# Optimization experiments

Measured on AMD Instinct MI355X. Metric: run time of the kernel, lower is better.

## Reference

```python
import jax, jax.numpy as jnp
from jax import lax
import numpy as np

FS = 48000
N_CHANNELS = 40
LOW_FREQ = 50
BATCH = 8
T_SAMPLES = 96000  # 2 s at 48 kHz
DOWN_FACTOR = 24   # 48 kHz -> 2 kHz envelope rate


def make_erb_fcoefs(fs, n_channels, low_freq):
    """Port of make_ERB_filters (Slaney gammatone coefficients). (C, 10)."""
    T = 1.0 / fs
    EarQ, minBW = 9.26449, 24.7
    i = np.arange(1, n_channels + 1, dtype=np.float64)
    hi = fs / 2
    cf = -(EarQ * minBW) + np.exp(i * (-np.log(hi + EarQ * minBW) + np.log(low_freq + EarQ * minBW)) / n_channels) * (hi + EarQ * minBW)
    erb = cf / EarQ + minBW
    B = 1.019 * 2 * np.pi * erb
    c = np.cos(2 * cf * np.pi * T)
    s = np.sin(2 * cf * np.pi * T)
    e = np.exp(B * T)
    sp = np.sqrt(3 + 2 ** 1.5)
    sm = np.sqrt(3 - 2 ** 1.5)
    a0 = T
    b1 = -2 * c / e
    b2 = np.exp(-2 * B * T)
    a11 = -(2 * T * c / e + 2 * sp * T * s / e) / 2
    a12 = -(2 * T * c / e - 2 * sp * T * s / e) / 2
    a13 = -(2 * T * c / e + 2 * sm * T * s / e) / 2
    a14 = -(2 * T * c / e - 2 * sm * T * s / e) / 2
    z = np.exp(4j * cf * np.pi * T)
    w = np.exp(-(B * T) + 2j * cf * np.pi * T)
    gain = np.abs(
        (-2 * z * T + 2 * w * T * (c - sm * s)) *
        (-2 * z * T + 2 * w * T * (c + sm * s)) *
        (-2 * z * T + 2 * w * T * (c - sp * s)) *
        (-2 * z * T + 2 * w * T * (c + sp * s)) /
        (-2 / np.exp(2 * B * T) - 2 * z + 2 * (1 + z) / np.exp(B * T)) ** 4)
    fcoefs = np.stack([np.full_like(cf, a0), a11, a12, a13, a14,
                       np.zeros_like(cf), np.ones_like(cf), b1, b2, gain], axis=1)
    return fcoefs.astype(np.float32)


def setup_inputs() -> dict:
    key = jax.random.key(0)
    x = jax.random.normal(key, (BATCH, T_SAMPLES), dtype=jnp.float32)
    fcoefs = jnp.asarray(make_erb_fcoefs(FS, N_CHANNELS, LOW_FREQ))
    return {"x": x, "fcoefs": fcoefs}


def _erb_filter_bank(x, fcoefs):
    """Cascaded 4-stage biquad gammatone bank. x: (B, T) -> (B, C, T)."""
    C = fcoefs.shape[0]
    Bsz = x.shape[0]
    a0 = fcoefs[:, 0]
    a2 = fcoefs[:, 5]  # zeros
    gain = fcoefs[:, 9]
    # numerator coeffs per stage, (4, 3, C); stage 1 divided by gain
    num = jnp.stack([
        jnp.stack([a0 / gain, fcoefs[:, 1] / gain, a2 / gain]),
        jnp.stack([a0, fcoefs[:, 2], a2]),
        jnp.stack([a0, fcoefs[:, 3], a2]),
        jnp.stack([a0, fcoefs[:, 4], a2]),
    ])
    d1 = fcoefs[:, 7]  # denominator (b0 == 1)
    d2 = fcoefs[:, 8]

    def step(carry, xt):
        s1, s2 = carry  # each (4, B, C): DF-II-transposed states per stage
        xk = jnp.broadcast_to(xt[:, None], (Bsz, C))
        ns1, ns2 = [], []
        for k in range(4):
            y = num[k, 0] * xk + s1[k]
            ns1.append(num[k, 1] * xk - d1 * y + s2[k])
            ns2.append(num[k, 2] * xk - d2 * y)
            xk = y
        return (jnp.stack(ns1), jnp.stack(ns2)), xk

    s0 = jnp.zeros((4, Bsz, C), x.dtype)
    _, ys = lax.scan(step, (s0, s0), x.T)  # ys: (T, B, C)
    return jnp.transpose(ys, (1, 2, 0))    # (B, C, T)


def reference(x, fcoefs):
    sub = _erb_filter_bank(x, fcoefs)          # (B, C, T)
    sub = jax.nn.relu(sub)                      # half-wave rectification
    Bsz, C, T = sub.shape
    env = sub.reshape(Bsz, C, T // DOWN_FACTOR, DOWN_FACTOR).mean(-1)  # avg-pool downsample
    return env  # (B, C, T/DOWN_FACTOR)
```

## Files before the change

### kernel.cpp

```cpp
#include <hip/hip_runtime.h>


#define NCH  40
#define NB   8
#define TS   96000
#define DOWN 24
#define NSEG 256
#define SEG  375
#define TD   4000
#define NLVL 8
#define INV24 (1.0f/24.0f)

typedef double DMat[4][4][2][2];

__device__ __forceinline__ void dmatcopy(DMat dst, const DMat src) {
    #pragma unroll
    for (int i = 0; i < 4; i++)
        #pragma unroll
        for (int j = 0; j < 4; j++) if (j <= i)
            #pragma unroll
            for (int r = 0; r < 2; r++)
                #pragma unroll
                for (int c = 0; c < 2; c++)
                    dst[i][j][r][c] = src[i][j][r][c];
}

__device__ __forceinline__ void dmatmul(DMat C, const DMat A, const DMat B) {
    #pragma unroll
    for (int i = 0; i < 4; i++)
        #pragma unroll
        for (int j = 0; j < 4; j++) if (j <= i)
            #pragma unroll
            for (int r = 0; r < 2; r++)
                #pragma unroll
                for (int c = 0; c < 2; c++) {
                    double acc = 0.0;
                    #pragma unroll
                    for (int k = 0; k < 4; k++) if (k >= j && k <= i)
                        #pragma unroll
                        for (int q = 0; q < 2; q++)
                            acc += A[i][k][r][q] * B[k][j][q][c];
                    C[i][j][r][c] = acc;
                }
}

__global__ __launch_bounds__(64)
void cochlea_setup(const float* __restrict__ fcoefs, double* __restrict__ ws)
{
    const int c = (int)threadIdx.x;
    if (c >= NCH) return;
    const float* fc = fcoefs + c * 10;
    const double a0  = (double)fc[0];
    const double n11 = (double)fc[2], n12 = (double)fc[3], n13 = (double)fc[4];
    const double nd1 = -(double)fc[7], nd2 = -(double)fc[8];

    double s[8];
    auto step0 = [&]() {
        double y0 = s[0];
        s[0] = nd1 * y0 + s[1];
        s[1] = nd2 * y0;
        double y1 = a0 * y0 + s[2];
        s[2] = nd1 * y1 + (n11 * y0 + s[3]);
        s[3] = nd2 * y1;
        double y2 = a0 * y1 + s[4];
        s[4] = nd1 * y2 + (n12 * y1 + s[5]);
        s[5] = nd2 * y2;
        double y3 = a0 * y2 + s[6];
        s[6] = nd1 * y3 + (n13 * y2 + s[7]);
        s[7] = nd2 * y3;
    };

    DMat A, P, T;
    #pragma unroll
    for (int j = 0; j < 8; j++) {
        #pragma unroll
        for (int i = 0; i < 8; i++) s[i] = (i == j) ? 1.0 : 0.0;
        step0();
        #pragma unroll
        for (int i = 0; i < 8; i++)
            if ((i >> 1) >= (j >> 1))
                A[i >> 1][j >> 1][i & 1][j & 1] = s[i];
    }

    dmatcopy(P, A);
    const int bits[8] = {0, 1, 1, 1, 0, 1, 1, 1};
    #pragma unroll
    for (int t = 0; t < 8; t++) {
        dmatmul(T, P, P);
        if (bits[t]) dmatmul(P, T, A);
        else         dmatcopy(P, T);
    }

    double* o = ws + (size_t)c * (NLVL * 40);
    for (int k = 0; k < NLVL; k++) {
        #pragma unroll
        for (int rb = 0; rb < 4; rb++)
            #pragma unroll
            for (int cb = 0; cb < 4; cb++) if (cb <= rb)
                #pragma unroll
                for (int ri = 0; ri < 2; ri++)
                    #pragma unroll
                    for (int ci = 0; ci < 2; ci++)
                        o[k * 40 + (rb * (rb + 1) / 2 + cb) * 4 + ri * 2 + ci] = P[rb][cb][ri][ci];
        if (k < NLVL - 1) { dmatmul(T, P, P); dmatcopy(P, T); }
    }
}

__global__ __launch_bounds__(256, 1)
void cochlea_main(const float* __restrict__ x,
                  const float* __restrict__ fcoefs,
                  const double* __restrict__ ws,
                  float* __restrict__ out)
{
    const int b = (int)blockIdx.x;
    const int c = (int)blockIdx.y;
    const int g = (int)threadIdx.x;

    const float* fc  = fcoefs + c * 10;
    const float a0   = fc[0];
    const float gain = fc[9];
    const float n00  = a0 / gain;
    const float n10  = fc[1] / gain;
    const float n11  = fc[2];
    const float n12  = fc[3];
    const float n13  = fc[4];
    const float nd1  = -fc[7];
    const float nd2  = -fc[8];

    float s[8];
    auto step = [&](float xv) -> float {
        float y0 = fmaf(n00, xv, s[0]);
        s[0] = fmaf(nd1, y0, fmaf(n10, xv, s[1]));
        s[1] = nd2 * y0;
        float y1 = fmaf(a0, y0, s[2]);
        s[2] = fmaf(nd1, y1, fmaf(n11, y0, s[3]));
        s[3] = nd2 * y1;
        float y2 = fmaf(a0, y1, s[4]);
        s[4] = fmaf(nd1, y2, fmaf(n12, y1, s[5]));
        s[5] = nd2 * y2;
        float y3 = fmaf(a0, y2, s[6]);
        s[6] = fmaf(nd1, y3, fmaf(n13, y2, s[7]));
        s[7] = nd2 * y3;
        return y3;
    };

    const float3* xb3 = reinterpret_cast<const float3*>(x + (size_t)b * TS + (size_t)g * SEG);
    float3 bA[5], bB[5];
    auto loadg = [&](float3 (&bf)[5], int m) {
        #pragma unroll
        for (int q = 0; q < 5; q++) bf[q] = xb3[m * 5 + q];
    };

    #pragma unroll
    for (int i = 0; i < 8; i++) s[i] = 0.f;
    auto c1 = [&](const float3 (&bf)[5]) {
        #pragma unroll
        for (int q = 0; q < 5; q++) { step(bf[q].x); step(bf[q].y); step(bf[q].z); }
    };
    loadg(bA, 0);
    for (int p = 0; p < 12; p++) {
        loadg(bB, 2 * p + 1);
        c1(bA);
        loadg(bA, 2 * p + 2);
        c1(bB);
    }
    c1(bA);

    __shared__ double tk[2][NSEG][9];
    double td[8];
    #pragma unroll
    for (int i = 0; i < 8; i++) td[i] = (double)s[i];
    int cur = 0;
    #pragma unroll
    for (int i = 0; i < 8; i++) tk[0][g][i] = td[i];
    __syncthreads();

    const double* wsc = ws + (size_t)c * (NLVL * 40);
    for (int k = 0; k < NLVL; k++) {
        double M[40];
        #pragma unroll
        for (int q = 0; q < 40; q++) M[q] = wsc[k * 40 + q];
        double nt[8];
        const int src = g - (1 << k);
        if (src >= 0) {
            double pr[8];
            #pragma unroll
            for (int i = 0; i < 8; i++) pr[i] = tk[cur][src][i];
            #pragma unroll
            for (int rb = 0; rb < 4; rb++)
                #pragma unroll
                for (int ri = 0; ri < 2; ri++) {
                    double acc = td[2 * rb + ri];
                    #pragma unroll
                    for (int cb = 0; cb < 4; cb++) if (cb <= rb)
                        #pragma unroll
                        for (int ci = 0; ci < 2; ci++)
                            acc += M[(rb * (rb + 1) / 2 + cb) * 4 + ri * 2 + ci] * pr[2 * cb + ci];
                    nt[2 * rb + ri] = acc;
                }
        } else {
            #pragma unroll
            for (int i = 0; i < 8; i++) nt[i] = td[i];
        }
        #pragma unroll
        for (int i = 0; i < 8; i++) tk[cur ^ 1][g][i] = nt[i];
        __syncthreads();
        #pragma unroll
        for (int i = 0; i < 8; i++) td[i] = nt[i];
        cur ^= 1;
    }

    #pragma unroll
    for (int i = 0; i < 8; i++)
        s[i] = (g == 0) ? 0.f : (float)tk[cur][g - 1][i];

    const int g8      = g & 7;
    const int offset  = (15 * g8) % 24;
    const int r       = (24 - offset) % 24;
    const bool hashead = (offset != 0);
    const int w0      = (SEG * g + r) / 24;
    const int ph      = (1 + 5 * g8) & 7;
    float* outp = out + ((size_t)b * NCH + c) * TD;

    float acc = 0.f, head = 0.f;
    int kb = 0;

    auto c2 = [&](const float3 (&bf)[5], int m) {
        #pragma unroll
        for (int q = 0; q < 5; q++) {
            float3 v = bf[q];
            acc += fmaxf(step(v.x), 0.f);
            acc += fmaxf(step(v.y), 0.f);
            acc += fmaxf(step(v.z), 0.f);
            int jj = m * 5 + q;
            if (((jj + ph) & 7) == 0) {
                bool ishead = hashead && (kb == 0);
                if (ishead) head = acc;
                else        outp[w0 + kb - (hashead ? 1 : 0)] = acc * INV24;
                kb++;
                acc = 0.f;
            }
        }
    };
    loadg(bA, 0);
    for (int p = 0; p < 12; p++) {
        loadg(bB, 2 * p + 1);
        c2(bA, 2 * p);
        loadg(bA, 2 * p + 2);
        c2(bB, 2 * p + 1);
    }
    c2(bA, 24);

    float hnext = __shfl_down(head, 1, 64);
    if (g8 != 7)
        outp[w0 + kb - (hashead ? 1 : 0)] = (acc + hnext) * INV24;
}

extern "C" void kernel_launch(void* const* d_in, const int* in_sizes, int n_in,
                              void* d_out, int out_size, void* d_ws, size_t ws_size,
                              hipStream_t stream) {
    const float* x      = (const float*)d_in[0];
    const float* fcoefs = (const float*)d_in[1];
    float* out = (float*)d_out;
    double* ws = (double*)d_ws;

    cochlea_setup<<<1, 64, 0, stream>>>(fcoefs, ws);
    dim3 grid(NB, NCH);
    cochlea_main<<<grid, 256, 0, stream>>>(x, fcoefs, ws, out);
}
```

Measured before the change: 122.2 us.

## Process two time segments per thread with packed float2 FMA recurrences

Each thread now runs two independent segments (g and g+128) of the IIR recurrence at once, using 2-wide float vectors so the compiler can emit packed FMA instructions. The block shrinks from 256 to 128 threads, and each thread does two matrix-vector updates per level in the double-precision scan. The aim is to double arithmetic throughput per instruction on the serial recurrence. In exchange, the two interleaved chains raise register pressure per thread and leave half as many waves to hide latency.

```diff
diff --git a/kernel.cpp b/kernel.cpp
--- a/kernel.cpp
+++ b/kernel.cpp
@@ -1,5 +1,7 @@
 #include <hip/hip_runtime.h>
 
+
+typedef float f32x2 __attribute__((ext_vector_type(2)));
 
 #define NCH  40
 #define NB   8
@@ -7,6 +9,7 @@
 #define DOWN 24
 #define NSEG 256
 #define SEG  375
+#define HALF 128
 #define TD   4000
 #define NLVL 8
 #define INV24 (1.0f/24.0f)
@@ -106,7 +109,7 @@
     }
 }
 
-__global__ __launch_bounds__(256, 1)
+__global__ __launch_bounds__(128, 1)
 void cochlea_main(const float* __restrict__ x,
                   const float* __restrict__ fcoefs,
                   const double* __restrict__ ws,
@@ -121,58 +124,70 @@
     const float gain = fc[9];
     const float n00  = a0 / gain;
     const float n10  = fc[1] / gain;
-    const float n11  = fc[2];
-    const float n12  = fc[3];
-    const float n13  = fc[4];
-    const float nd1  = -fc[7];
-    const float nd2  = -fc[8];
-
-    float s[8];
-    auto step = [&](float xv) -> float {
-        float y0 = fmaf(n00, xv, s[0]);
-        s[0] = fmaf(nd1, y0, fmaf(n10, xv, s[1]));
-        s[1] = nd2 * y0;
-        float y1 = fmaf(a0, y0, s[2]);
-        s[2] = fmaf(nd1, y1, fmaf(n11, y0, s[3]));
-        s[3] = nd2 * y1;
-        float y2 = fmaf(a0, y1, s[4]);
-        s[4] = fmaf(nd1, y2, fmaf(n12, y1, s[5]));
-        s[5] = nd2 * y2;
-        float y3 = fmaf(a0, y2, s[6]);
-        s[6] = fmaf(nd1, y3, fmaf(n13, y2, s[7]));
-        s[7] = nd2 * y3;
+
+    const f32x2 va0  = {a0, a0};
+    const f32x2 vn00 = {n00, n00};
+    const f32x2 vn10 = {n10, n10};
+    const f32x2 vn11 = {fc[2], fc[2]};
+    const f32x2 vn12 = {fc[3], fc[3]};
+    const f32x2 vn13 = {fc[4], fc[4]};
+    const f32x2 vnd1 = {-fc[7], -fc[7]};
+    const f32x2 vnd2 = {-fc[8], -fc[8]};
+    const f32x2 vz   = {0.f, 0.f};
+
+    f32x2 S[8];
+    auto stepp = [&](f32x2 xv) -> f32x2 {
+        f32x2 y0 = __builtin_elementwise_fma(vn00, xv, S[0]);
+        S[0] = __builtin_elementwise_fma(vnd1, y0, __builtin_elementwise_fma(vn10, xv, S[1]));
+        S[1] = vnd2 * y0;
+        f32x2 y1 = __builtin_elementwise_fma(va0, y0, S[2]);
+        S[2] = __builtin_elementwise_fma(vnd1, y1, __builtin_elementwise_fma(vn11, y0, S[3]));
+        S[3] = vnd2 * y1;
+        f32x2 y2 = __builtin_elementwise_fma(va0, y1, S[4]);
+        S[4] = __builtin_elementwise_fma(vnd1, y2, __builtin_elementwise_fma(vn12, y1, S[5]));
+        S[5] = vnd2 * y2;
+        f32x2 y3 = __builtin_elementwise_fma(va0, y2, S[6]);
+        S[6] = __builtin_elementwise_fma(vnd1, y3, __builtin_elementwise_fma(vn13, y2, S[7]));
+        S[7] = vnd2 * y3;
         return y3;
     };
-
-    const float3* xb3 = reinterpret_cast<const float3*>(x + (size_t)b * TS + (size_t)g * SEG);
-    float3 bA[5], bB[5];
-    auto loadg = [&](float3 (&bf)[5], int m) {
-        #pragma unroll
-        for (int q = 0; q < 5; q++) bf[q] = xb3[m * 5 + q];
-    };
-
-    #pragma unroll
-    for (int i = 0; i < 8; i++) s[i] = 0.f;
-    auto c1 = [&](const float3 (&bf)[5]) {
-        #pragma unroll
-        for (int q = 0; q < 5; q++) { step(bf[q].x); step(bf[q].y); step(bf[q].z); }
-    };
-    loadg(bA, 0);
+    auto mk2 = [](float u, float v) { f32x2 r; r.x = u; r.y = v; return r; };
+
+    const float* xb = x + (size_t)b * TS;
+    const float3* xa3 = reinterpret_cast<const float3*>(xb + (size_t)g * SEG);
+    const float3* xc3 = reinterpret_cast<const float3*>(xb + (size_t)(g + HALF) * SEG);
+    float3 aA[5], cA[5], aB[5], cB[5];
+    auto loadg = [&](float3 (&fa)[5], float3 (&fb)[5], int m) {
+        #pragma unroll
+        for (int q = 0; q < 5; q++) { fa[q] = xa3[m * 5 + q]; fb[q] = xc3[m * 5 + q]; }
+    };
+
+    #pragma unroll
+    for (int i = 0; i < 8; i++) S[i] = vz;
+    auto c1 = [&](const float3 (&fa)[5], const float3 (&fb)[5]) {
+        #pragma unroll
+        for (int q = 0; q < 5; q++) {
+            stepp(mk2(fa[q].x, fb[q].x));
+            stepp(mk2(fa[q].y, fb[q].y));
+            stepp(mk2(fa[q].z, fb[q].z));
+        }
+    };
+    loadg(aA, cA, 0);
     for (int p = 0; p < 12; p++) {
-        loadg(bB, 2 * p + 1);
-        c1(bA);
-        loadg(bA, 2 * p + 2);
-        c1(bB);
-    }
-    c1(bA);
+        loadg(aB, cB, 2 * p + 1);
+        c1(aA, cA);
+        loadg(aA, cA, 2 * p + 2);
+        c1(aB, cB);
+    }
+    c1(aA, cA);
 
     __shared__ double tk[2][NSEG][9];
-    double td[8];
-    #pragma unroll
-    for (int i = 0; i < 8; i++) td[i] = (double)s[i];
+    double tdx[8], tdy[8];
+    #pragma unroll
+    for (int i = 0; i < 8; i++) { tdx[i] = (double)S[i].x; tdy[i] = (double)S[i].y; }
     int cur = 0;
     #pragma unroll
-    for (int i = 0; i < 8; i++) tk[0][g][i] = td[i];
+    for (int i = 0; i < 8; i++) { tk[0][g][i] = tdx[i]; tk[0][g + HALF][i] = tdy[i]; }
     __syncthreads();
 
     const double* wsc = ws + (size_t)c * (NLVL * 40);
@@ -180,12 +195,12 @@
         double M[40];
         #pragma unroll
         for (int q = 0; q < 40; q++) M[q] = wsc[k * 40 + q];
-        double nt[8];
-        const int src = g - (1 << k);
-        if (src >= 0) {
+
+        auto matvec = [&](double (&td)[8], int src) {
             double pr[8];
             #pragma unroll
             for (int i = 0; i < 8; i++) pr[i] = tk[cur][src][i];
+            double nt[8];
             #pragma unroll
             for (int rb = 0; rb < 4; rb++)
                 #pragma unroll
@@ -198,62 +213,74 @@
                             acc += M[(rb * (rb + 1) / 2 + cb) * 4 + ri * 2 + ci] * pr[2 * cb + ci];
                     nt[2 * rb + ri] = acc;
                 }
-        } else {
-            #pragma unroll
-            for (int i = 0; i < 8; i++) nt[i] = td[i];
-        }
-        #pragma unroll
-        for (int i = 0; i < 8; i++) tk[cur ^ 1][g][i] = nt[i];
+            #pragma unroll
+            for (int i = 0; i < 8; i++) td[i] = nt[i];
+        };
+
+        const int d = 1 << k;
+        if (g - d >= 0) matvec(tdx, g - d);
+        matvec(tdy, g + HALF - d);
+
+        #pragma unroll
+        for (int i = 0; i < 8; i++) { tk[cur ^ 1][g][i] = tdx[i]; tk[cur ^ 1][g + HALF][i] = tdy[i]; }
         __syncthreads();
-        #pragma unroll
-        for (int i = 0; i < 8; i++) td[i] = nt[i];
         cur ^= 1;
     }
 
     #pragma unroll
-    for (int i = 0; i < 8; i++)
-        s[i] = (g == 0) ? 0.f : (float)tk[cur][g - 1][i];
+    for (int i = 0; i < 8; i++) {
+        S[i].x = (g == 0) ? 0.f : (float)tk[cur][g - 1][i];
+        S[i].y = (float)tk[cur][g + HALF - 1][i];
+    }
 
     const int g8      = g & 7;
     const int offset  = (15 * g8) % 24;
     const int r       = (24 - offset) % 24;
     const bool hashead = (offset != 0);
+    const int hh      = hashead ? 1 : 0;
     const int w0      = (SEG * g + r) / 24;
     const int ph      = (1 + 5 * g8) & 7;
     float* outp = out + ((size_t)b * NCH + c) * TD;
 
-    float acc = 0.f, head = 0.f;
+    f32x2 acc = vz, head = vz;
     int kb = 0;
 
-    auto c2 = [&](const float3 (&bf)[5], int m) {
+    auto c2 = [&](const float3 (&fa)[5], const float3 (&fb)[5], int m) {
         #pragma unroll
         for (int q = 0; q < 5; q++) {
-            float3 v = bf[q];
-            acc += fmaxf(step(v.x), 0.f);
-            acc += fmaxf(step(v.y), 0.f);
-            acc += fmaxf(step(v.z), 0.f);
+            acc += __builtin_elementwise_max(stepp(mk2(fa[q].x, fb[q].x)), vz);
+            acc += __builtin_elementwise_max(stepp(mk2(fa[q].y, fb[q].y)), vz);
+            acc += __builtin_elementwise_max(stepp(mk2(fa[q].z, fb[q].z)), vz);
             int jj = m * 5 + q;
             if (((jj + ph) & 7) == 0) {
                 bool ishead = hashead && (kb == 0);
                 if (ishead) head = acc;
-                else        outp[w0 + kb - (hashead ? 1 : 0)] = acc * INV24;
+                else {
+                    int idx = w0 + kb - hh;
+                    outp[idx]        = acc.x * INV24;
+                    outp[idx + 2000] = acc.y * INV24;
+                }
                 kb++;
-                acc = 0.f;
+                acc = vz;
             }
         }
     };
-    loadg(bA, 0);
+    loadg(aA, cA, 0);
     for (int p = 0; p < 12; p++) {
-        loadg(bB, 2 * p + 1);
-        c2(bA, 2 * p);
-        loadg(bA, 2 * p + 2);
-        c2(bB, 2 * p + 1);
-    }
-    c2(bA, 24);
-
-    float hnext = __shfl_down(head, 1, 64);
-    if (g8 != 7)
-        outp[w0 + kb - (hashead ? 1 : 0)] = (acc + hnext) * INV24;
+        loadg(aB, cB, 2 * p + 1);
+        c2(aA, cA, 2 * p);
+        loadg(aA, cA, 2 * p + 2);
+        c2(aB, cB, 2 * p + 1);
+    }
+    c2(aA, cA, 24);
+
+    float hx = __shfl_down(head.x, 1, 64);
+    float hy = __shfl_down(head.y, 1, 64);
+    if (g8 != 7) {
+        int idx = w0 + kb - hh;
+        outp[idx]        = (acc.x + hx) * INV24;
+        outp[idx + 2000] = (acc.y + hy) * INV24;
+    }
 }
 
 extern "C" void kernel_launch(void* const* d_in, const int* in_sizes, int n_in,
@@ -266,5 +293,5 @@
 
     cochlea_setup<<<1, 64, 0, stream>>>(fcoefs, ws);
     dim3 grid(NB, NCH);
-    cochlea_main<<<grid, 256, 0, stream>>>(x, fcoefs, ws, out);
-}
+    cochlea_main<<<grid, 128, 0, stream>>>(x, fcoefs, ws, out);
+}
```

Result: slower. 181.5 us (+48.5%).

## Process two channels per thread with packed float2 FMA

Applied to the files above, without the earlier changes.

Each block now handles a pair of channels (c and c+20), carrying both filter states in 2-wide float vectors so the recurrence can use packed FMA instructions and share the input loads. The grid shrinks from 320 to 160 blocks, and the double-precision carry scan runs twice in sequence, once per channel. This trades parallelism and occupancy (fewer blocks on a large GPU) for higher per-thread instruction throughput and half the input traffic.

```diff
diff --git a/kernel.cpp b/kernel.cpp
--- a/kernel.cpp
+++ b/kernel.cpp
@@ -1,8 +1,11 @@
 #include <hip/hip_runtime.h>
 
+
+typedef float f32x2 __attribute__((ext_vector_type(2)));
 
 #define NCH  40
 #define NB   8
+#define NCP  20
 #define TS   96000
 #define DOWN 24
 #define NSEG 256
@@ -112,35 +115,39 @@
                   const double* __restrict__ ws,
                   float* __restrict__ out)
 {
-    const int b = (int)blockIdx.x;
-    const int c = (int)blockIdx.y;
-    const int g = (int)threadIdx.x;
-
-    const float* fc  = fcoefs + c * 10;
-    const float a0   = fc[0];
-    const float gain = fc[9];
-    const float n00  = a0 / gain;
-    const float n10  = fc[1] / gain;
-    const float n11  = fc[2];
-    const float n12  = fc[3];
-    const float n13  = fc[4];
-    const float nd1  = -fc[7];
-    const float nd2  = -fc[8];
-
-    float s[8];
-    auto step = [&](float xv) -> float {
-        float y0 = fmaf(n00, xv, s[0]);
-        s[0] = fmaf(nd1, y0, fmaf(n10, xv, s[1]));
-        s[1] = nd2 * y0;
-        float y1 = fmaf(a0, y0, s[2]);
-        s[2] = fmaf(nd1, y1, fmaf(n11, y0, s[3]));
-        s[3] = nd2 * y1;
-        float y2 = fmaf(a0, y1, s[4]);
-        s[4] = fmaf(nd1, y2, fmaf(n12, y1, s[5]));
-        s[5] = nd2 * y2;
-        float y3 = fmaf(a0, y2, s[6]);
-        s[6] = fmaf(nd1, y3, fmaf(n13, y2, s[7]));
-        s[7] = nd2 * y3;
+    const int b  = (int)blockIdx.x;
+    const int cp = (int)blockIdx.y;
+    const int g  = (int)threadIdx.x;
+
+    const float* fA = fcoefs + cp * 10;
+    const float* fB = fcoefs + (cp + NCP) * 10;
+
+    auto mk2 = [](float u, float v) { f32x2 r; r.x = u; r.y = v; return r; };
+    const f32x2 va0  = mk2(fA[0], fB[0]);
+    const f32x2 vn00 = mk2(fA[0] / fA[9], fB[0] / fB[9]);
+    const f32x2 vn10 = mk2(fA[1] / fA[9], fB[1] / fB[9]);
+    const f32x2 vn11 = mk2(fA[2], fB[2]);
+    const f32x2 vn12 = mk2(fA[3], fB[3]);
+    const f32x2 vn13 = mk2(fA[4], fB[4]);
+    const f32x2 vnd1 = mk2(-fA[7], -fB[7]);
+    const f32x2 vnd2 = mk2(-fA[8], -fB[8]);
+    const f32x2 vz   = mk2(0.f, 0.f);
+
+    f32x2 S[8];
+    auto stepp = [&](float xu) -> f32x2 {
+        f32x2 xv = mk2(xu, xu);
+        f32x2 y0 = __builtin_elementwise_fma(vn00, xv, S[0]);
+        S[0] = __builtin_elementwise_fma(vnd1, y0, __builtin_elementwise_fma(vn10, xv, S[1]));
+        S[1] = vnd2 * y0;
+        f32x2 y1 = __builtin_elementwise_fma(va0, y0, S[2]);
+        S[2] = __builtin_elementwise_fma(vnd1, y1, __builtin_elementwise_fma(vn11, y0, S[3]));
+        S[3] = vnd2 * y1;
+        f32x2 y2 = __builtin_elementwise_fma(va0, y1, S[4]);
+        S[4] = __builtin_elementwise_fma(vnd1, y2, __builtin_elementwise_fma(vn12, y1, S[5]));
+        S[5] = vnd2 * y2;
+        f32x2 y3 = __builtin_elementwise_fma(va0, y2, S[6]);
+        S[6] = __builtin_elementwise_fma(vnd1, y3, __builtin_elementwise_fma(vn13, y2, S[7]));
+        S[7] = vnd2 * y3;
         return y3;
     };
 
@@ -152,10 +159,10 @@
     };
 
     #pragma unroll
-    for (int i = 0; i < 8; i++) s[i] = 0.f;
+    for (int i = 0; i < 8; i++) S[i] = vz;
     auto c1 = [&](const float3 (&bf)[5]) {
         #pragma unroll
-        for (int q = 0; q < 5; q++) { step(bf[q].x); step(bf[q].y); step(bf[q].z); }
+        for (int q = 0; q < 5; q++) { stepp(bf[q].x); stepp(bf[q].y); stepp(bf[q].z); }
     };
     loadg(bA, 0);
     for (int p = 0; p < 12; p++) {
@@ -167,78 +174,95 @@
     c1(bA);
 
     __shared__ double tk[2][NSEG][9];
-    double td[8];
-    #pragma unroll
-    for (int i = 0; i < 8; i++) td[i] = (double)s[i];
-    int cur = 0;
-    #pragma unroll
-    for (int i = 0; i < 8; i++) tk[0][g][i] = td[i];
-    __syncthreads();
-
-    const double* wsc = ws + (size_t)c * (NLVL * 40);
-    for (int k = 0; k < NLVL; k++) {
-        double M[40];
-        #pragma unroll
-        for (int q = 0; q < 40; q++) M[q] = wsc[k * 40 + q];
-        double nt[8];
-        const int src = g - (1 << k);
-        if (src >= 0) {
-            double pr[8];
-            #pragma unroll
-            for (int i = 0; i < 8; i++) pr[i] = tk[cur][src][i];
-            #pragma unroll
-            for (int rb = 0; rb < 4; rb++)
-                #pragma unroll
-                for (int ri = 0; ri < 2; ri++) {
-                    double acc = td[2 * rb + ri];
+    float iA[8], iB[8];
+
+    auto run_scan = [&](const double* wsc, const double (&ei)[8], float (&oi)[8]) {
+        int cur = 0;
+        #pragma unroll
+        for (int i = 0; i < 8; i++) tk[0][g][i] = ei[i];
+        __syncthreads();
+        double td[8];
+        #pragma unroll
+        for (int i = 0; i < 8; i++) td[i] = ei[i];
+        for (int k = 0; k < NLVL; k++) {
+            double M[40];
+            #pragma unroll
+            for (int q = 0; q < 40; q++) M[q] = wsc[k * 40 + q];
+            const int d = 1 << k;
+            if (g >= d) {
+                double pr[8];
+                #pragma unroll
+                for (int i = 0; i < 8; i++) pr[i] = tk[cur][g - d][i];
+                double nt[8];
+                #pragma unroll
+                for (int rb = 0; rb < 4; rb++)
                     #pragma unroll
-                    for (int cb = 0; cb < 4; cb++) if (cb <= rb)
+                    for (int ri = 0; ri < 2; ri++) {
+                        double acc = td[2 * rb + ri];
                         #pragma unroll
-                        for (int ci = 0; ci < 2; ci++)
-                            acc += M[(rb * (rb + 1) / 2 + cb) * 4 + ri * 2 + ci] * pr[2 * cb + ci];
-                    nt[2 * rb + ri] = acc;
-                }
-        } else {
-            #pragma unroll
-            for (int i = 0; i < 8; i++) nt[i] = td[i];
+                        for (int cb = 0; cb < 4; cb++) if (cb <= rb)
+                            #pragma unroll
+                            for (int ci = 0; ci < 2; ci++)
+                                acc += M[(rb * (rb + 1) / 2 + cb) * 4 + ri * 2 + ci] * pr[2 * cb + ci];
+                        nt[2 * rb + ri] = acc;
+                    }
+                #pragma unroll
+                for (int i = 0; i < 8; i++) td[i] = nt[i];
+            }
+            #pragma unroll
+            for (int i = 0; i < 8; i++) tk[cur ^ 1][g][i] = td[i];
+            __syncthreads();
+            cur ^= 1;
         }
         #pragma unroll
-        for (int i = 0; i < 8; i++) tk[cur ^ 1][g][i] = nt[i];
+        for (int i = 0; i < 8; i++) oi[i] = (g == 0) ? 0.f : (float)tk[cur][g - 1][i];
         __syncthreads();
-        #pragma unroll
-        for (int i = 0; i < 8; i++) td[i] = nt[i];
-        cur ^= 1;
-    }
-
-    #pragma unroll
-    for (int i = 0; i < 8; i++)
-        s[i] = (g == 0) ? 0.f : (float)tk[cur][g - 1][i];
+    };
+
+    {
+        double e[8];
+        #pragma unroll
+        for (int i = 0; i < 8; i++) e[i] = (double)S[i].x;
+        run_scan(ws + (size_t)cp * (NLVL * 40), e, iA);
+        #pragma unroll
+        for (int i = 0; i < 8; i++) e[i] = (double)S[i].y;
+        run_scan(ws + (size_t)(cp + NCP) * (NLVL * 40), e, iB);
+    }
+
+    #pragma unroll
+    for (int i = 0; i < 8; i++) S[i] = mk2(iA[i], iB[i]);
 
     const int g8      = g & 7;
     const int offset  = (15 * g8) % 24;
     const int r       = (24 - offset) % 24;
     const bool hashead = (offset != 0);
+    const int hh      = hashead ? 1 : 0;
     const int w0      = (SEG * g + r) / 24;
     const int ph      = (1 + 5 * g8) & 7;
-    float* outp = out + ((size_t)b * NCH + c) * TD;
-
-    float acc = 0.f, head = 0.f;
+    float* outA = out + ((size_t)b * NCH + cp) * TD;
+    float* outB = out + ((size_t)b * NCH + cp + NCP) * TD;
+
+    f32x2 acc = vz, head = vz;
     int kb = 0;
 
     auto c2 = [&](const float3 (&bf)[5], int m) {
         #pragma unroll
         for (int q = 0; q < 5; q++) {
             float3 v = bf[q];
-            acc += fmaxf(step(v.x), 0.f);
-            acc += fmaxf(step(v.y), 0.f);
-            acc += fmaxf(step(v.z), 0.f);
+            acc += __builtin_elementwise_max(stepp(v.x), vz);
+            acc += __builtin_elementwise_max(stepp(v.y), vz);
+            acc += __builtin_elementwise_max(stepp(v.z), vz);
             int jj = m * 5 + q;
             if (((jj + ph) & 7) == 0) {
                 bool ishead = hashead && (kb == 0);
                 if (ishead) head = acc;
-                else        outp[w0 + kb - (hashead ? 1 : 0)] = acc * INV24;
+                else {
+                    int idx = w0 + kb - hh;
+                    outA[idx] = acc.x * INV24;
+                    outB[idx] = acc.y * INV24;
+                }
                 kb++;
-                acc = 0.f;
+                acc = vz;
             }
         }
     };
@@ -251,9 +275,13 @@
     }
     c2(bA, 24);
 
-    float hnext = __shfl_down(head, 1, 64);
-    if (g8 != 7)
-        outp[w0 + kb - (hashead ? 1 : 0)] = (acc + hnext) * INV24;
+    float hx = __shfl_down(head.x, 1, 64);
+    float hy = __shfl_down(head.y, 1, 64);
+    if (g8 != 7) {
+        int idx = w0 + kb - hh;
+        outA[idx] = (acc.x + hx) * INV24;
+        outB[idx] = (acc.y + hy) * INV24;
+    }
 }
 
 extern "C" void kernel_launch(void* const* d_in, const int* in_sizes, int n_in,
@@ -265,6 +293,6 @@
     double* ws = (double*)d_ws;
 
     cochlea_setup<<<1, 64, 0, stream>>>(fcoefs, ws);
-    dim3 grid(NB, NCH);
+    dim3 grid(NB, NCP);
     cochlea_main<<<grid, 256, 0, stream>>>(x, fcoefs, ws, out);
 }
```

After: 113.6 us. 1.08x faster.
